# Optimization experiments

Measured on AMD Instinct MI355X. Metric: run time of the kernel, lower is better.

The kernel has to match this reference:

```python
import jax, jax.numpy as jnp
import numpy as np

N_NODES = 50000


def setup_inputs() -> dict:
    key = jax.random.key(0)
    k1, k2, k3, k4, k5 = jax.random.split(key, 5)
    x = jax.random.normal(k1, (N_NODES, 128), dtype=jnp.float32)
    edge_index = jax.random.randint(k2, (2, 800000), 0, N_NODES, dtype=jnp.int64)
    # Linear layers: torch Linear stores weight as [out, in]; init ~ U(-1/sqrt(in), 1/sqrt(in))
    s = 1.0 / np.sqrt(128.0)
    W_rel = jax.random.uniform(k3, (128, 128), dtype=jnp.float32, minval=-s, maxval=s)
    b_rel = jax.random.uniform(k4, (128,), dtype=jnp.float32, minval=-s, maxval=s)
    W_root = jax.random.uniform(k5, (128, 128), dtype=jnp.float32, minval=-s, maxval=s)
    return {"x": x, "edge_index": edge_index, "W_rel": W_rel, "b_rel": b_rel, "W_root": W_root}


def reference(x, edge_index, W_rel, b_rel, W_root):
    # GraphConv (PyG): out_i = W_rel @ (sum_{j -> i} x_j) + b_rel + W_root @ x_i
    src, dst = edge_index[0], edge_index[1]
    msgs = x[src]  # [E, in] gather
    agg = jax.ops.segment_sum(msgs, dst, num_segments=N_NODES)  # [N, in] scatter-add
    out = agg @ W_rel.T + b_rel + x @ W_root.T
    # ReLU; dropout_rate = DropoutRate.NONE -> p=0, identity
    return jax.nn.relu(out)
```

## Files before the change

kernel.cpp:

```cpp
#include <hip/hip_runtime.h>
#include <hip/hip_bf16.h>
#include <hip/hip_cooperative_groups.h>

namespace cg = cooperative_groups;


#define F 128
#define NPB 32
#define NPARTS 8
#define CAP 128
#define CAPB 768
#define AST 68

typedef __bf16 bf16x8 __attribute__((ext_vector_type(8)));
typedef float f32x4 __attribute__((ext_vector_type(4)));

__device__ inline unsigned f32_to_bf16_rne(float f) {
  unsigned u = __float_as_uint(f);
  unsigned r = u + 0x7fffu + ((u >> 16) & 1u);
  return r >> 16;
}
__device__ inline unsigned pack2(float2 v) {
  return f32_to_bf16_rne(v.x) | (f32_to_bf16_rne(v.y) << 16);
}
__device__ inline void upk(unsigned v, float& ax, float& ay) {
  ax += __uint_as_float(v << 16);
  ay += __uint_as_float(v & 0xffff0000u);
}

__global__ __launch_bounds__(256) void mega_kernel(
    const float2* __restrict__ x, const float2* __restrict__ w0,
    const float2* __restrict__ w1, const int* __restrict__ ei,
    unsigned* __restrict__ xb, unsigned* __restrict__ wb,
    int* __restrict__ binCursor, unsigned* __restrict__ bin,
    const float* __restrict__ brel, float* __restrict__ out,
    int N, int E, int NB, int n2x, int n2w) {
  cg::grid_group grid = cg::this_grid();
  const int t = threadIdx.x;
  const int b = blockIdx.x;
  const int gtid = b * 256 + t;
  const int gstride = gridDim.x * 256;

  for (int i = gtid; i < NPARTS * NB; i += gstride) binCursor[i] = 0;
  for (int i = gtid; i < n2x; i += gstride) xb[i] = pack2(x[i]);
  for (int i = gtid; i < 2 * n2w; i += gstride)
    wb[i] = (i < n2w) ? pack2(w0[i]) : pack2(w1[i - n2w]);
  grid.sync();

  const int part = b & (NPARTS - 1);
  for (int e = gtid; e < E; e += gstride) {
    unsigned src = (unsigned)ei[e];
    unsigned dst = (unsigned)ei[E + e];
    int cell = part * NB + (int)(dst >> 5);
    int slot = atomicAdd(&binCursor[cell], 1);
    if (slot < CAP) bin[(size_t)cell * CAP + slot] = (dst << 16) | src;
  }
  grid.sync();

  __shared__ int cntS[NPB];
  __shared__ int offS[NPB];
  __shared__ int curS[NPB];
  __shared__ unsigned short eLds[CAPB];
  __shared__ unsigned aLds[NPB * AST];

  if (t < NPB) cntS[t] = 0;
  __syncthreads();

  unsigned kreg[NPARTS];
  int cnt_p[NPARTS];
#pragma unroll
  for (int p = 0; p < NPARTS; ++p) {
    int cell = p * NB + b;
    int c = min(binCursor[cell], CAP);
    cnt_p[p] = c;
    kreg[p] = (t < c) ? bin[(size_t)cell * CAP + t] : 0u;
  }
#pragma unroll
  for (int p = 0; p < NPARTS; ++p) {
    if (t < cnt_p[p]) atomicAdd(&cntS[(kreg[p] >> 16) & (NPB - 1)], 1);
  }
  __syncthreads();

  if (t < 64) {
    int v = (t < NPB) ? cntS[t] : 0;
    int incl = v;
#pragma unroll
    for (int off = 1; off < NPB; off <<= 1) {
      int u = __shfl_up(incl, off);
      if (t >= off) incl += u;
    }
    if (t < NPB) {
      offS[t] = incl - v;
      curS[t] = incl - v;
    }
  }
  __syncthreads();

#pragma unroll
  for (int p = 0; p < NPARTS; ++p) {
    if (t < cnt_p[p]) {
      int d = (kreg[p] >> 16) & (NPB - 1);
      int pos = atomicAdd(&curS[d], 1);
      if (pos < CAPB) eLds[pos] = (unsigned short)(kreg[p] & 0xffffu);
    }
  }
  __syncthreads();

  const int wave = t >> 6;
  const int lane = t & 63;
  const int nodeBase = b * NPB;
#pragma unroll
  for (int di = wave; di < NPB; di += 4) {
    float ax = 0.f, ay = 0.f;
    int beg = min(offS[di], CAPB);
    int end = min(offS[di] + cntS[di], CAPB);
    int e = beg;
    for (; e + 7 < end; e += 8) {
      int s0 = eLds[e + 0];
      int s1 = eLds[e + 1];
      int s2 = eLds[e + 2];
      int s3 = eLds[e + 3];
      int s4 = eLds[e + 4];
      int s5 = eLds[e + 5];
      int s6 = eLds[e + 6];
      int s7 = eLds[e + 7];
      unsigned v0 = xb[(size_t)s0 * 64 + lane];
      unsigned v1 = xb[(size_t)s1 * 64 + lane];
      unsigned v2 = xb[(size_t)s2 * 64 + lane];
      unsigned v3 = xb[(size_t)s3 * 64 + lane];
      unsigned v4 = xb[(size_t)s4 * 64 + lane];
      unsigned v5 = xb[(size_t)s5 * 64 + lane];
      unsigned v6 = xb[(size_t)s6 * 64 + lane];
      unsigned v7 = xb[(size_t)s7 * 64 + lane];
      upk(v0, ax, ay);
      upk(v1, ax, ay);
      upk(v2, ax, ay);
      upk(v3, ax, ay);
      upk(v4, ax, ay);
      upk(v5, ax, ay);
      upk(v6, ax, ay);
      upk(v7, ax, ay);
    }
    for (; e + 3 < end; e += 4) {
      int s0 = eLds[e + 0];
      int s1 = eLds[e + 1];
      int s2 = eLds[e + 2];
      int s3 = eLds[e + 3];
      unsigned v0 = xb[(size_t)s0 * 64 + lane];
      unsigned v1 = xb[(size_t)s1 * 64 + lane];
      unsigned v2 = xb[(size_t)s2 * 64 + lane];
      unsigned v3 = xb[(size_t)s3 * 64 + lane];
      upk(v0, ax, ay);
      upk(v1, ax, ay);
      upk(v2, ax, ay);
      upk(v3, ax, ay);
    }
    for (; e < end; ++e) upk(xb[(size_t)eLds[e] * 64 + lane], ax, ay);
    aLds[di * AST + lane] = f32_to_bf16_rne(ax) | (f32_to_bf16_rne(ay) << 16);
  }
  __syncthreads();

  const int m16 = lane & 15;
  const int quad = lane >> 4;
  const f32x4 zero4 = {0.f, 0.f, 0.f, 0.f};
  const bf16x8 zero8 = {};
  f32x4 acc[2][2];
#pragma unroll
  for (int mt = 0; mt < 2; ++mt)
#pragma unroll
    for (int s = 0; s < 2; ++s) acc[mt][s] = zero4;

  const __bf16* __restrict__ wbb = (const __bf16*)wb;
#pragma unroll
  for (int ph = 0; ph < 2; ++ph) {
    const __bf16* __restrict__ W = wbb + (size_t)ph * F * F;
#pragma unroll
    for (int k0 = 0; k0 < F; k0 += 32) {
      const int kcol = k0 + 8 * quad;
      bf16x8 a[2], bw[2];
#pragma unroll
      for (int mt = 0; mt < 2; ++mt) {
        if (ph == 0) {
          a[mt] = *(const bf16x8*)&aLds[(mt * 16 + m16) * AST + (kcol >> 1)];
        } else {
          int row = nodeBase + mt * 16 + m16;
          a[mt] = (row < N)
                      ? *(const bf16x8*)((const __bf16*)xb + (size_t)row * F + kcol)
                      : zero8;
        }
      }
#pragma unroll
      for (int s = 0; s < 2; ++s) {
        int nt = wave * 2 + s;
        bw[s] = *(const bf16x8*)(W + (size_t)(nt * 16 + m16) * F + kcol);
      }
#pragma unroll
      for (int mt = 0; mt < 2; ++mt)
#pragma unroll
        for (int s = 0; s < 2; ++s)
          acc[mt][s] = __builtin_amdgcn_mfma_f32_16x16x32_bf16(
              a[mt], bw[s], acc[mt][s], 0, 0, 0);
    }
  }

#pragma unroll
  for (int s = 0; s < 2; ++s) {
    int nt = wave * 2 + s;
    float bias = brel[nt * 16 + m16];
#pragma unroll
    for (int mt = 0; mt < 2; ++mt) {
      int row0 = nodeBase + mt * 16 + quad * 4;
#pragma unroll
      for (int r = 0; r < 4; ++r) {
        int row = row0 + r;
        if (row < N)
          out[(size_t)row * F + nt * 16 + m16] = fmaxf(acc[mt][s][r] + bias, 0.f);
      }
    }
  }
}

__global__ __launch_bounds__(256) void prep_bin_kernel(
    const float2* __restrict__ x, const float2* __restrict__ w0,
    const float2* __restrict__ w1, const int* __restrict__ ei,
    unsigned* __restrict__ xb, unsigned* __restrict__ wb,
    int* __restrict__ binCursor, unsigned* __restrict__ bin,
    int E, int NB, int n2x, int n2w) {
  const int tid0 = blockIdx.x * blockDim.x + threadIdx.x;
  const int stride = gridDim.x * blockDim.x;
  const int totalc = n2x + 2 * n2w;
  for (int i = tid0; i < totalc; i += stride) {
    if (i < n2x) xb[i] = pack2(x[i]);
    else if (i < n2x + n2w) wb[i - n2x] = pack2(w0[i - n2x]);
    else wb[i - n2x] = pack2(w1[i - n2x - n2w]);
  }
  const int part = blockIdx.x & (NPARTS - 1);
  for (int e = tid0; e < E; e += stride) {
    unsigned src = (unsigned)ei[e];
    unsigned dst = (unsigned)ei[E + e];
    int cell = part * NB + (int)(dst >> 5);
    int slot = atomicAdd(&binCursor[cell], 1);
    if (slot < CAP) bin[(size_t)cell * CAP + slot] = (dst << 16) | src;
  }
}

__global__ __launch_bounds__(256) void agg_gemm_kernel(
    const unsigned* __restrict__ xb, const unsigned* __restrict__ bin,
    const int* __restrict__ binCursor, const __bf16* __restrict__ wb,
    const float* __restrict__ brel, float* __restrict__ out, int N, int NB) {
  __shared__ int cntS[NPB];
  __shared__ int offS[NPB];
  __shared__ int curS[NPB];
  __shared__ unsigned short eLds[CAPB];
  __shared__ unsigned aLds[NPB * AST];
  const int b = blockIdx.x;
  const int t = threadIdx.x;
  if (t < NPB) cntS[t] = 0;
  __syncthreads();
  unsigned kreg[NPARTS];
  int cnt_p[NPARTS];
#pragma unroll
  for (int p = 0; p < NPARTS; ++p) {
    int cell = p * NB + b;
    int c = min(binCursor[cell], CAP);
    cnt_p[p] = c;
    kreg[p] = (t < c) ? bin[(size_t)cell * CAP + t] : 0u;
  }
#pragma unroll
  for (int p = 0; p < NPARTS; ++p) {
    if (t < cnt_p[p]) atomicAdd(&cntS[(kreg[p] >> 16) & (NPB - 1)], 1);
  }
  __syncthreads();
  if (t < 64) {
    int v = (t < NPB) ? cntS[t] : 0;
    int incl = v;
#pragma unroll
    for (int off = 1; off < NPB; off <<= 1) {
      int u = __shfl_up(incl, off);
      if (t >= off) incl += u;
    }
    if (t < NPB) {
      offS[t] = incl - v;
      curS[t] = incl - v;
    }
  }
  __syncthreads();
#pragma unroll
  for (int p = 0; p < NPARTS; ++p) {
    if (t < cnt_p[p]) {
      int d = (kreg[p] >> 16) & (NPB - 1);
      int pos = atomicAdd(&curS[d], 1);
      if (pos < CAPB) eLds[pos] = (unsigned short)(kreg[p] & 0xffffu);
    }
  }
  __syncthreads();
  const int wave = t >> 6;
  const int lane = t & 63;
  const int nodeBase = b * NPB;
#pragma unroll
  for (int di = wave; di < NPB; di += 4) {
    float ax = 0.f, ay = 0.f;
    int beg = min(offS[di], CAPB);
    int end = min(offS[di] + cntS[di], CAPB);
    int e = beg;
    for (; e + 3 < end; e += 4) {
      int s0 = eLds[e + 0];
      int s1 = eLds[e + 1];
      int s2 = eLds[e + 2];
      int s3 = eLds[e + 3];
      unsigned v0 = xb[(size_t)s0 * 64 + lane];
      unsigned v1 = xb[(size_t)s1 * 64 + lane];
      unsigned v2 = xb[(size_t)s2 * 64 + lane];
      unsigned v3 = xb[(size_t)s3 * 64 + lane];
      upk(v0, ax, ay);
      upk(v1, ax, ay);
      upk(v2, ax, ay);
      upk(v3, ax, ay);
    }
    for (; e < end; ++e) upk(xb[(size_t)eLds[e] * 64 + lane], ax, ay);
    aLds[di * AST + lane] = f32_to_bf16_rne(ax) | (f32_to_bf16_rne(ay) << 16);
  }
  __syncthreads();
  const int m16 = lane & 15;
  const int quad = lane >> 4;
  const f32x4 zero4 = {0.f, 0.f, 0.f, 0.f};
  const bf16x8 zero8 = {};
  f32x4 acc[2][2];
#pragma unroll
  for (int mt = 0; mt < 2; ++mt)
#pragma unroll
    for (int s = 0; s < 2; ++s) acc[mt][s] = zero4;
#pragma unroll
  for (int ph = 0; ph < 2; ++ph) {
    const __bf16* __restrict__ W = wb + (size_t)ph * F * F;
#pragma unroll
    for (int k0 = 0; k0 < F; k0 += 32) {
      const int kcol = k0 + 8 * quad;
      bf16x8 a[2], bw[2];
#pragma unroll
      for (int mt = 0; mt < 2; ++mt) {
        if (ph == 0) {
          a[mt] = *(const bf16x8*)&aLds[(mt * 16 + m16) * AST + (kcol >> 1)];
        } else {
          int row = nodeBase + mt * 16 + m16;
          a[mt] = (row < N)
                      ? *(const bf16x8*)((const __bf16*)xb + (size_t)row * F + kcol)
                      : zero8;
        }
      }
#pragma unroll
      for (int s = 0; s < 2; ++s) {
        int nt = wave * 2 + s;
        bw[s] = *(const bf16x8*)(W + (size_t)(nt * 16 + m16) * F + kcol);
      }
#pragma unroll
      for (int mt = 0; mt < 2; ++mt)
#pragma unroll
        for (int s = 0; s < 2; ++s)
          acc[mt][s] = __builtin_amdgcn_mfma_f32_16x16x32_bf16(
              a[mt], bw[s], acc[mt][s], 0, 0, 0);
    }
  }
#pragma unroll
  for (int s = 0; s < 2; ++s) {
    int nt = wave * 2 + s;
    float bias = brel[nt * 16 + m16];
#pragma unroll
    for (int mt = 0; mt < 2; ++mt) {
      int row0 = nodeBase + mt * 16 + quad * 4;
#pragma unroll
      for (int r = 0; r < 4; ++r) {
        int row = row0 + r;
        if (row < N)
          out[(size_t)row * F + nt * 16 + m16] = fmaxf(acc[mt][s][r] + bias, 0.f);
      }
    }
  }
}

__global__ __launch_bounds__(256) void scatter_add_kernel(
    const float4* __restrict__ x4, const int* __restrict__ ei,
    float* __restrict__ agg, int E) {
  int gid = blockIdx.x * blockDim.x + threadIdx.x;
  if (gid >= E * 32) return;
  int e = gid >> 5, q = gid & 31;
  float4 v = x4[(size_t)ei[e] * 32 + q];
  float* a = agg + (size_t)ei[E + e] * F + q * 4;
  atomicAdd(a + 0, v.x);
  atomicAdd(a + 1, v.y);
  atomicAdd(a + 2, v.z);
  atomicAdd(a + 3, v.w);
}

#define ROWS_PER_BLOCK 64
#define SA_STRIDE 36
#define SW_STRIDE 132

__global__ __launch_bounds__(256) void gemm_fused_kernel(
    const float* __restrict__ agg, const float* __restrict__ x,
    const float* __restrict__ Wrel, const float* __restrict__ Wroot,
    const float* __restrict__ brel, float* __restrict__ out, int N) {
  __shared__ float sA[ROWS_PER_BLOCK * SA_STRIDE];
  __shared__ float sW[32 * SW_STRIDE];
  const int tid = threadIdx.x;
  const int j0 = (tid & 31) * 4;
  const int r0 = (tid >> 5) * 8;
  const int rowBase = blockIdx.x * ROWS_PER_BLOCK;
  float acc[8][4];
#pragma unroll
  for (int r = 0; r < 8; ++r)
#pragma unroll
    for (int c = 0; c < 4; ++c) acc[r][c] = 0.0f;
  for (int phase = 0; phase < 2; ++phase) {
    const float* __restrict__ A = phase ? x : agg;
    const float* __restrict__ W = phase ? Wroot : Wrel;
    for (int kc = 0; kc < F; kc += 32) {
#pragma unroll
      for (int idx = tid; idx < 512; idx += 256) {
        int row = idx >> 3, k4 = idx & 7;
        float4 v = make_float4(0.f, 0.f, 0.f, 0.f);
        int grow = rowBase + row;
        if (grow < N) v = *(const float4*)&A[(size_t)grow * F + kc + k4 * 4];
        *(float4*)&sA[row * SA_STRIDE + k4 * 4] = v;
      }
#pragma unroll
      for (int idx = tid; idx < 4096; idx += 256) {
        int j = idx >> 5, kk = idx & 31;
        sW[kk * SW_STRIDE + j] = W[j * F + kc + kk];
      }
      __syncthreads();
#pragma unroll
      for (int kk = 0; kk < 32; ++kk) {
        float4 w = *(const float4*)&sW[kk * SW_STRIDE + j0];
#pragma unroll
        for (int r = 0; r < 8; ++r) {
          float a = sA[(r0 + r) * SA_STRIDE + kk];
          acc[r][0] = fmaf(a, w.x, acc[r][0]);
          acc[r][1] = fmaf(a, w.y, acc[r][1]);
          acc[r][2] = fmaf(a, w.z, acc[r][2]);
          acc[r][3] = fmaf(a, w.w, acc[r][3]);
        }
      }
      __syncthreads();
    }
  }
  float b0 = brel[j0], b1 = brel[j0 + 1], b2 = brel[j0 + 2], b3 = brel[j0 + 3];
#pragma unroll
  for (int r = 0; r < 8; ++r) {
    int row = rowBase + r0 + r;
    if (row < N) {
      float4 v;
      v.x = fmaxf(acc[r][0] + b0, 0.0f);
      v.y = fmaxf(acc[r][1] + b1, 0.0f);
      v.z = fmaxf(acc[r][2] + b2, 0.0f);
      v.w = fmaxf(acc[r][3] + b3, 0.0f);
      *(float4*)&out[(size_t)row * F + j0] = v;
    }
  }
}

extern "C" void kernel_launch(void* const* d_in, const int* in_sizes, int n_in,
                              void* d_out, int out_size, void* d_ws, size_t ws_size,
                              hipStream_t stream) {
  const float* x     = (const float*)d_in[0];
  const int*   ei    = (const int*)d_in[1];
  const float* Wrel  = (const float*)d_in[2];
  const float* brel  = (const float*)d_in[3];
  const float* Wroot = (const float*)d_in[4];
  float* out = (float*)d_out;

  const int N = in_sizes[0] / F;
  const int E = in_sizes[1] / 2;
  const int NB = (N + NPB - 1) / NPB;

  size_t xbBytes  = ((size_t)N * F * 2 + 255) & ~(size_t)255;
  size_t wBytes   = ((size_t)2 * F * F * 2 + 255) & ~(size_t)255;
  size_t curBytes = ((size_t)NPARTS * NB * sizeof(int) + 255) & ~(size_t)255;
  size_t binBytes = ((size_t)NPARTS * NB * CAP * sizeof(unsigned) + 255) & ~(size_t)255;
  size_t needBin  = curBytes + binBytes + xbBytes + wBytes;

  if (ws_size >= needBin) {
    int*      binCursor = (int*)d_ws;
    unsigned* bin = (unsigned*)((char*)d_ws + curBytes);
    unsigned* xb  = (unsigned*)((char*)d_ws + curBytes + binBytes);
    unsigned* wb  = (unsigned*)((char*)d_ws + curBytes + binBytes + xbBytes);

    int n2x = N * (F / 2);
    int n2w = F * F / 2;

    int maxBlocksPerCU = 0;
    hipError_t qerr = hipOccupancyMaxActiveBlocksPerMultiprocessor(
        &maxBlocksPerCU, (const void*)mega_kernel, 256, 0);
    bool coopOk = (qerr == hipSuccess) && (maxBlocksPerCU * 256 >= NB);

    if (coopOk) {
      const float2* xa = (const float2*)x;
      const float2* w0 = (const float2*)Wrel;
      const float2* w1 = (const float2*)Wroot;
      void* args[] = {(void*)&xa, (void*)&w0, (void*)&w1, (void*)&ei,
                      (void*)&xb, (void*)&wb, (void*)&binCursor, (void*)&bin,
                      (void*)&brel, (void*)&out,
                      (void*)&N, (void*)&E, (void*)&NB, (void*)&n2x, (void*)&n2w};
      hipError_t lerr = hipLaunchCooperativeKernel(
          (const void*)mega_kernel, dim3(NB), dim3(256), args, 0, stream);
      if (lerr == hipSuccess) return;
    }

    hipMemsetAsync(binCursor, 0, (size_t)NPARTS * NB * sizeof(int), stream);
    prep_bin_kernel<<<2048, 256, 0, stream>>>(
        (const float2*)x, (const float2*)Wrel, (const float2*)Wroot, ei, xb, wb,
        binCursor, bin, E, NB, n2x, n2w);
    agg_gemm_kernel<<<NB, 256, 0, stream>>>(xb, bin, binCursor,
                                            (const __bf16*)wb, brel, out, N, NB);
  } else {
    hipMemsetAsync(out, 0, (size_t)N * F * sizeof(float), stream);
    long long total = (long long)E * 32;
    scatter_add_kernel<<<(int)((total + 255) / 256), 256, 0, stream>>>(
        (const float4*)x, ei, out, E);
    gemm_fused_kernel<<<(N + ROWS_PER_BLOCK - 1) / ROWS_PER_BLOCK, 256, 0,
                        stream>>>(out, x, Wrel, Wroot, brel, out, N);
  }
}
```

Measured before the change: 171.8 us.

## Drop first grid sync, vectorize bf16 conversion and gather with 16B loads

Moves the bin-cursor zeroing to a host memset so the first grid-wide sync can be removed, and overlaps the fp32-to-bf16 conversion of x and weights with edge binning before the single remaining sync. Conversion now reads float4 and writes uint2. The neighbour gather has each 16-lane group load a full 256-byte row with uint4 loads, handling four edges in parallel per wave, then reduces across groups with shuffles. A launch-bounds occupancy hint is added. The costs are an extra memset launch and shuffle reductions, and the hint may limit registers.

```diff
diff --git a/kernel.cpp b/kernel.cpp
--- a/kernel.cpp
+++ b/kernel.cpp
@@ -23,29 +23,36 @@
 __device__ inline unsigned pack2(float2 v) {
   return f32_to_bf16_rne(v.x) | (f32_to_bf16_rne(v.y) << 16);
 }
+__device__ inline unsigned pack2f(float a, float b) {
+  return f32_to_bf16_rne(a) | (f32_to_bf16_rne(b) << 16);
+}
 __device__ inline void upk(unsigned v, float& ax, float& ay) {
   ax += __uint_as_float(v << 16);
   ay += __uint_as_float(v & 0xffff0000u);
 }
-
-__global__ __launch_bounds__(256) void mega_kernel(
-    const float2* __restrict__ x, const float2* __restrict__ w0,
+__device__ inline void upk4(uint4 v, float* a) {
+  a[0] += __uint_as_float(v.x << 16);
+  a[1] += __uint_as_float(v.x & 0xffff0000u);
+  a[2] += __uint_as_float(v.y << 16);
+  a[3] += __uint_as_float(v.y & 0xffff0000u);
+  a[4] += __uint_as_float(v.z << 16);
+  a[5] += __uint_as_float(v.z & 0xffff0000u);
+  a[6] += __uint_as_float(v.w << 16);
+  a[7] += __uint_as_float(v.w & 0xffff0000u);
+}
+
+__global__ __launch_bounds__(256, 7) void mega_kernel(
+    const float4* __restrict__ x, const float2* __restrict__ w0,
     const float2* __restrict__ w1, const int* __restrict__ ei,
     unsigned* __restrict__ xb, unsigned* __restrict__ wb,
     int* __restrict__ binCursor, unsigned* __restrict__ bin,
     const float* __restrict__ brel, float* __restrict__ out,
-    int N, int E, int NB, int n2x, int n2w) {
+    int N, int E, int NB, int n4x, int n2w) {
   cg::grid_group grid = cg::this_grid();
   const int t = threadIdx.x;
   const int b = blockIdx.x;
   const int gtid = b * 256 + t;
   const int gstride = gridDim.x * 256;
-
-  for (int i = gtid; i < NPARTS * NB; i += gstride) binCursor[i] = 0;
-  for (int i = gtid; i < n2x; i += gstride) xb[i] = pack2(x[i]);
-  for (int i = gtid; i < 2 * n2w; i += gstride)
-    wb[i] = (i < n2w) ? pack2(w0[i]) : pack2(w1[i - n2w]);
-  grid.sync();
 
   const int part = b & (NPARTS - 1);
   for (int e = gtid; e < E; e += gstride) {
@@ -55,6 +62,13 @@
     int slot = atomicAdd(&binCursor[cell], 1);
     if (slot < CAP) bin[(size_t)cell * CAP + slot] = (dst << 16) | src;
   }
+  uint2* __restrict__ xb2 = (uint2*)xb;
+  for (int i = gtid; i < n4x; i += gstride) {
+    float4 v = x[i];
+    xb2[i] = make_uint2(pack2f(v.x, v.y), pack2f(v.z, v.w));
+  }
+  for (int i = gtid; i < 2 * n2w; i += gstride)
+    wb[i] = (i < n2w) ? pack2(w0[i]) : pack2(w1[i - n2w]);
   grid.sync();
 
   __shared__ int cntS[NPB];
@@ -108,55 +122,63 @@
 
   const int wave = t >> 6;
   const int lane = t & 63;
+  const int grp = lane >> 4;
+  const int l16 = lane & 15;
+  const uint4* __restrict__ xb4 = (const uint4*)xb;
   const int nodeBase = b * NPB;
-#pragma unroll
   for (int di = wave; di < NPB; di += 4) {
-    float ax = 0.f, ay = 0.f;
+    float a8[8] = {0.f, 0.f, 0.f, 0.f, 0.f, 0.f, 0.f, 0.f};
     int beg = min(offS[di], CAPB);
     int end = min(offS[di] + cntS[di], CAPB);
     int e = beg;
-    for (; e + 7 < end; e += 8) {
-      int s0 = eLds[e + 0];
-      int s1 = eLds[e + 1];
-      int s2 = eLds[e + 2];
-      int s3 = eLds[e + 3];
-      int s4 = eLds[e + 4];
-      int s5 = eLds[e + 5];
-      int s6 = eLds[e + 6];
-      int s7 = eLds[e + 7];
-      unsigned v0 = xb[(size_t)s0 * 64 + lane];
-      unsigned v1 = xb[(size_t)s1 * 64 + lane];
-      unsigned v2 = xb[(size_t)s2 * 64 + lane];
-      unsigned v3 = xb[(size_t)s3 * 64 + lane];
-      unsigned v4 = xb[(size_t)s4 * 64 + lane];
-      unsigned v5 = xb[(size_t)s5 * 64 + lane];
-      unsigned v6 = xb[(size_t)s6 * 64 + lane];
-      unsigned v7 = xb[(size_t)s7 * 64 + lane];
-      upk(v0, ax, ay);
-      upk(v1, ax, ay);
-      upk(v2, ax, ay);
-      upk(v3, ax, ay);
-      upk(v4, ax, ay);
-      upk(v5, ax, ay);
-      upk(v6, ax, ay);
-      upk(v7, ax, ay);
-    }
-    for (; e + 3 < end; e += 4) {
-      int s0 = eLds[e + 0];
-      int s1 = eLds[e + 1];
-      int s2 = eLds[e + 2];
-      int s3 = eLds[e + 3];
-      unsigned v0 = xb[(size_t)s0 * 64 + lane];
-      unsigned v1 = xb[(size_t)s1 * 64 + lane];
-      unsigned v2 = xb[(size_t)s2 * 64 + lane];
-      unsigned v3 = xb[(size_t)s3 * 64 + lane];
-      upk(v0, ax, ay);
-      upk(v1, ax, ay);
-      upk(v2, ax, ay);
-      upk(v3, ax, ay);
-    }
-    for (; e < end; ++e) upk(xb[(size_t)eLds[e] * 64 + lane], ax, ay);
-    aLds[di * AST + lane] = f32_to_bf16_rne(ax) | (f32_to_bf16_rne(ay) << 16);
+    for (; e + 16 <= end; e += 16) {
+      int s0 = eLds[e + grp];
+      int s1 = eLds[e + 4 + grp];
+      int s2 = eLds[e + 8 + grp];
+      int s3 = eLds[e + 12 + grp];
+      uint4 v0 = xb4[(size_t)s0 * 16 + l16];
+      uint4 v1 = xb4[(size_t)s1 * 16 + l16];
+      uint4 v2 = xb4[(size_t)s2 * 16 + l16];
+      uint4 v3 = xb4[(size_t)s3 * 16 + l16];
+      upk4(v0, a8);
+      upk4(v1, a8);
+      upk4(v2, a8);
+      upk4(v3, a8);
+    }
+    if (e + 8 <= end) {
+      int s0 = eLds[e + grp];
+      int s1 = eLds[e + 4 + grp];
+      uint4 v0 = xb4[(size_t)s0 * 16 + l16];
+      uint4 v1 = xb4[(size_t)s1 * 16 + l16];
+      upk4(v0, a8);
+      upk4(v1, a8);
+      e += 8;
+    }
+    if (e < end) {
+      int i0 = e + grp;
+      int i1 = e + 4 + grp;
+      if (i0 < end) {
+        uint4 v0 = xb4[(size_t)eLds[i0] * 16 + l16];
+        upk4(v0, a8);
+      }
+      if (i1 < end) {
+        uint4 v1 = xb4[(size_t)eLds[i1] * 16 + l16];
+        upk4(v1, a8);
+      }
+    }
+#pragma unroll
+    for (int j = 0; j < 8; ++j) {
+      a8[j] += __shfl_xor(a8[j], 16);
+      a8[j] += __shfl_xor(a8[j], 32);
+    }
+    if (grp == 0) {
+      uint4 pk;
+      pk.x = pack2f(a8[0], a8[1]);
+      pk.y = pack2f(a8[2], a8[3]);
+      pk.z = pack2f(a8[4], a8[5]);
+      pk.w = pack2f(a8[6], a8[7]);
+      *((uint4*)&aLds[di * AST + l16 * 4]) = pk;
+    }
   }
   __syncthreads();
 
@@ -486,6 +508,7 @@
     unsigned* wb  = (unsigned*)((char*)d_ws + curBytes + binBytes + xbBytes);
 
     int n2x = N * (F / 2);
+    int n4x = N * (F / 4);
     int n2w = F * F / 2;
 
     int maxBlocksPerCU = 0;
@@ -494,13 +517,14 @@
     bool coopOk = (qerr == hipSuccess) && (maxBlocksPerCU * 256 >= NB);
 
     if (coopOk) {
-      const float2* xa = (const float2*)x;
+      hipMemsetAsync(binCursor, 0, (size_t)NPARTS * NB * sizeof(int), stream);
+      const float4* xa = (const float4*)x;
       const float2* w0 = (const float2*)Wrel;
       const float2* w1 = (const float2*)Wroot;
       void* args[] = {(void*)&xa, (void*)&w0, (void*)&w1, (void*)&ei,
                       (void*)&xb, (void*)&wb, (void*)&binCursor, (void*)&bin,
                       (void*)&brel, (void*)&out,
-                      (void*)&N, (void*)&E, (void*)&NB, (void*)&n2x, (void*)&n2w};
+                      (void*)&N, (void*)&E, (void*)&NB, (void*)&n4x, (void*)&n2w};
       hipError_t lerr = hipLaunchCooperativeKernel(
           (const void*)mega_kernel, dim3(NB), dim3(256), args, 0, stream);
       if (lerr == hipSuccess) return;
```

After: 171.6 us. No clear change (-0.1%).
